# Performance work log

Measured on AMD Instinct MI355X. Metric: run time of the kernel, lower is better.

Reference implementation:

```python
import jax, jax.numpy as jnp
import numpy as np

M_TOKENS = 4096   # flattened batch*seq
K_IN = 4096       # in_features
N_OUT = 11008     # out_features
GROUPSIZE = 128


def setup_inputs() -> dict:
    key = jax.random.key(0)
    k1, k2, k3 = jax.random.split(key, 3)
    x = jax.random.normal(k1, (M_TOKENS, K_IN), dtype=jnp.float32)
    # unpacked int4 codes in [0, 15], row-major [N, K] (logical weight layout)
    weight_q = jax.random.randint(k2, (N_OUT, K_IN), 0, 16, dtype=jnp.int32)
    # [K//G, N, 2]: [..., 0] = scales, [..., 1] = zeros (gpt-fast pack_scales_and_zeros layout)
    scales_and_zeros = jax.random.uniform(k3, (K_IN // GROUPSIZE, N_OUT, 2), dtype=jnp.float32)
    return {"x": x, "weight_q": weight_q, "scales_and_zeros": scales_and_zeros}


def reference(x, weight_q, scales_and_zeros):
    # Group-wise affine dequant: w[k, n] = (q[n, k] - 8) * scale[k//G, n] + zero[k//G, n]
    N, K = weight_q.shape
    n_groups = scales_and_zeros.shape[0]
    G = K // n_groups
    scales = scales_and_zeros[..., 0]  # [K//G, N]
    zeros = scales_and_zeros[..., 1]   # [K//G, N]
    q = weight_q.astype(x.dtype).T.reshape(n_groups, G, N)          # [K//G, G, N]
    w = (q - 8.0) * scales[:, None, :] + zeros[:, None, :]          # [K//G, G, N]
    w = w.reshape(K, N)
    return x @ w  # [M, N]
```

## Files before the change

kernel.cpp:

```cpp
#include <hip/hip_runtime.h>
#include <hip/hip_bf16.h>
#include <math.h>

#define M_TOKENS 4096
#define K_IN     4096
#define N_OUT    11008

#define BM 256
#define BN 256
#define BK 128
#define KTILES (K_IN / BK)

typedef int i32x4 __attribute__((ext_vector_type(4)));

__device__ __forceinline__ void async_copy16(const void* g, void* l) {
    __builtin_amdgcn_global_load_lds(
        (const __attribute__((address_space(1))) void*)g,
        (__attribute__((address_space(3))) void*)l, 16, 0, 0);
}

__global__ __launch_bounds__(256) void quant_x_kernel(const float* __restrict__ x,
                                                      char* __restrict__ xq,
                                                      float* __restrict__ xs) {
    __shared__ float wmax[4];
    const int m = blockIdx.x;
    const int t = threadIdx.x;
    const float* row = x + (size_t)m * K_IN;
    float4 v[4];
    float lmax = 0.f;
#pragma unroll
    for (int p = 0; p < 4; ++p) {
        v[p] = *reinterpret_cast<const float4*>(row + p * 1024 + t * 4);
        lmax = fmaxf(lmax, fmaxf(fmaxf(fabsf(v[p].x), fabsf(v[p].y)),
                                 fmaxf(fabsf(v[p].z), fabsf(v[p].w))));
    }
#pragma unroll
    for (int off = 32; off >= 1; off >>= 1)
        lmax = fmaxf(lmax, __shfl_xor(lmax, off, 64));
    if ((t & 63) == 0) wmax[t >> 6] = lmax;
    __syncthreads();
    float gmax = fmaxf(fmaxf(wmax[0], wmax[1]), fmaxf(wmax[2], wmax[3]));
    gmax = fmaxf(gmax, 1e-20f);
    const float inv = 127.f / gmax;
    if (t == 0) xs[m] = gmax / 127.f;
#pragma unroll
    for (int p = 0; p < 4; ++p) {
        float vv[4] = {v[p].x, v[p].y, v[p].z, v[p].w};
        alignas(4) char c[4];
#pragma unroll
        for (int j = 0; j < 4; ++j) {
            float q = rintf(vv[j] * inv);
            q = fminf(fmaxf(q, -127.f), 127.f);
            c[j] = (char)(int)q;
        }
        *reinterpret_cast<unsigned*>(xq + (size_t)m * K_IN + p * 1024 + t * 4) =
            *reinterpret_cast<const unsigned*>(c);
    }
}

__global__ __launch_bounds__(256) void scale_w_kernel(const float* __restrict__ snz,
                                                      float* __restrict__ ws,
                                                      float* __restrict__ wsinv) {
    int n = blockIdx.x * 256 + threadIdx.x;
    if (n >= N_OUT) return;
    float m = 0.f;
#pragma unroll 4
    for (int g = 0; g < 32; ++g) {
        float s = snz[((size_t)g * N_OUT + n) * 2];
        float z = snz[((size_t)g * N_OUT + n) * 2 + 1];
        m = fmaxf(m, fmaxf(fabsf(z - 8.f * s), fabsf(z + 7.f * s)));
    }
    m = fmaxf(m, 1e-20f);
    ws[n] = m / 127.f;
    wsinv[n] = 127.f / m;
}

__global__ __launch_bounds__(256) void dequant_kernel(const int* __restrict__ wq,
                                                      const float* __restrict__ snz,
                                                      const float* __restrict__ wsinv,
                                                      char* __restrict__ wb) {
    size_t idx = (size_t)blockIdx.x * 256 + threadIdx.x;
    int n  = (int)(idx >> 9);
    int k8 = (int)(idx & 511);
    int g  = k8 >> 4;
    const float* sz = snz + ((size_t)g * N_OUT + n) * 2;
    float scale = sz[0], zero = sz[1];
    float inv = wsinv[n];
    const int4* q4 = reinterpret_cast<const int4*>(wq + (size_t)n * K_IN + (size_t)k8 * 8);
    int4 qa = q4[0], qb = q4[1];
    int q[8] = {qa.x, qa.y, qa.z, qa.w, qb.x, qb.y, qb.z, qb.w};
    alignas(8) char t[8];
#pragma unroll
    for (int j = 0; j < 8; ++j) {
        float w = (float)(q[j] - 8) * scale + zero;
        float qq = rintf(w * inv);
        qq = fminf(fmaxf(qq, -127.f), 127.f);
        t[j] = (char)(int)qq;
    }
    *reinterpret_cast<uint2*>(wb + idx * 8) = *reinterpret_cast<const uint2*>(t);
}


#define SCB()  __builtin_amdgcn_sched_barrier(0)
#define SBAR() { SCB(); __builtin_amdgcn_s_barrier(); SCB(); }
#define LGKM0() { asm volatile("s_waitcnt lgkmcnt(0)" ::: "memory"); SCB(); }
#define VM4()  { asm volatile("s_waitcnt vmcnt(4)" ::: "memory"); SCB(); }

#define RD_AL(T, S) \
    _Pragma("unroll") for (int mi = 0; mi < 4; ++mi) aL[mi] = readA(T, mi, S);
#define RD_AH(T, S) \
    _Pragma("unroll") for (int mi = 0; mi < 4; ++mi) aH[mi] = readA(T, 4 + mi, S);
#define RD_B4(T, S) \
    _Pragma("unroll") for (int ni = 0; ni < 4; ++ni) bk[ni] = readB(T, ni, S);

#define MFMA16(AOFF, FRAG) \
    __builtin_amdgcn_s_setprio(1); \
    { \
        _Pragma("unroll") for (int mi = 0; mi < 4; ++mi) \
        _Pragma("unroll") for (int ni = 0; ni < 4; ++ni) \
            acc[AOFF + mi][ni] = __builtin_amdgcn_mfma_i32_16x16x64_i8( \
                FRAG[mi], bk[ni], acc[AOFF + mi][ni], 0, 0, 0); \
    } \
    __builtin_amdgcn_s_setprio(0);

#define TILE(CA, CB, NA, NB, K1, K2) \
     \
    RD_AL(CA, 0); RD_B4(CB, 0); \
    stageB(NB, K1, 1); \
    SBAR(); LGKM0(); \
    MFMA16(0, aL); \
    VM4(); SBAR();    \
     \
    RD_AH(CA, 0); \
    stageA(NA, K1, 0); \
    SBAR(); LGKM0(); \
    MFMA16(4, aH); \
    SBAR(); \
     \
    RD_AL(CA, 1); RD_B4(CB, 1); \
    stageA(NA, K1, 1); \
    SBAR(); LGKM0(); \
    MFMA16(0, aL); \
    SBAR(); \
     \
    RD_AH(CA, 1); \
    stageB(CB, K2, 0); \
    SBAR(); LGKM0(); \
    MFMA16(4, aH); \
    VM4(); SBAR();

__global__ __launch_bounds__(512, 2) void gemm_i8_kernel(
        const char* __restrict__ Xq,
        const char* __restrict__ Wq,
        const float* __restrict__ xs,
        const float* __restrict__ ws,
        float* __restrict__ C) {
    __shared__ alignas(16) char smem[131072];
    char* const ldsA = smem;
    char* const ldsB = smem + 65536;

    const int tid  = threadIdx.x;
    const int lane = tid & 63;
    const int wave = tid >> 6;
    const int wr   = wave >> 2;
    const int wc   = wave & 3;
    const int l15  = lane & 15;
    const int lrow = lane >> 3;
    const int ssw  = (((lane & 7) ^ lrow) << 4);

    unsigned bid = blockIdx.x;
    unsigned per = gridDim.x >> 3;
    unsigned swz = (bid & 7u) * per + (bid >> 3);
    const int tn = (int)(swz % (N_OUT / BN));
    const int tm = (int)(swz / (N_OUT / BN));
    const int m0 = tm * BM;
    const int n0 = tn * BN;

    const int colswz = (((lane >> 4) << 4) ^ ((lane & 7) << 4));

    i32x4 acc[8][4];
#pragma unroll
    for (int i = 0; i < 8; ++i)
#pragma unroll
        for (int j = 0; j < 4; ++j) {
            i32x4 z = {0, 0, 0, 0};
            acc[i][j] = z;
        }
    i32x4 aL[4], aH[4], bk[4];

    auto stageA = [&](char* dstTile, int kt, int unit) {
#pragma unroll
        for (int j = 0; j < 2; ++j) {
            int c  = wave * 2 + j;
            int rb = (c >> 3) * 128 + (c & 7) * 8 + unit * 64;
            const char* g = Xq + (size_t)(m0 + rb + lrow) * K_IN
                            + (size_t)kt * 128 + ssw;
            async_copy16(g, dstTile + rb * 128);
        }
    };
    auto stageB = [&](char* dstTile, int kt, int unit) {
#pragma unroll
        for (int j = 0; j < 2; ++j) {
            int c  = wave * 2 + j;
            int rb = (c >> 2) * 64 + (c & 3) * 8 + unit * 32;
            const char* g = Wq + (size_t)(n0 + rb + lrow) * K_IN
                            + (size_t)kt * 128 + ssw;
            async_copy16(g, dstTile + rb * 128);
        }
    };
    auto readA = [&](char* tile, int mi8, int s) -> i32x4 {
        return *(const i32x4*)(tile + (wr * 128 + mi8 * 16 + l15) * 128 + (colswz ^ (s << 6)));
    };
    auto readB = [&](char* tile, int ni4, int s) -> i32x4 {
        return *(const i32x4*)(tile + (wc * 64 + ni4 * 16 + l15) * 128 + (colswz ^ (s << 6)));
    };

    char* const A0 = ldsA;   char* const A1 = ldsA + 32768;
    char* const B0 = ldsB;   char* const B1 = ldsB + 32768;

    stageB(B0, 0, 0); stageB(B0, 0, 1); stageA(A0, 0, 0); stageA(A0, 0, 1);
    stageB(B1, 1, 0);
    VM4(); SBAR();

    for (int i = 0; i < KTILES / 2; ++i) {
        const int k1 = (2 * i + 1) & (KTILES - 1);
        const int k2 = (2 * i + 2) & (KTILES - 1);
        const int k3 = (2 * i + 3) & (KTILES - 1);
        TILE(A0, B0, A1, B1, k1, k2)
        TILE(A1, B1, A0, B0, k2, k3)
    }

    const int r4 = (lane >> 4) << 2;
    float sn[4];
#pragma unroll
    for (int nf = 0; nf < 4; ++nf) sn[nf] = ws[n0 + wc * 64 + nf * 16 + l15];
#pragma unroll
    for (int mi = 0; mi < 8; ++mi) {
        const float4 xm = *reinterpret_cast<const float4*>(xs + m0 + wr * 128 + mi * 16 + r4);
        const float xv[4] = {xm.x, xm.y, xm.z, xm.w};
#pragma unroll
        for (int nf = 0; nf < 4; ++nf)
#pragma unroll
            for (int e = 0; e < 4; ++e) {
                int row = m0 + wr * 128 + mi * 16 + r4 + e;
                int col = n0 + wc * 64 + nf * 16 + l15;
                C[(size_t)row * N_OUT + col] = (float)acc[mi][nf][e] * xv[e] * sn[nf];
            }
    }
}

extern "C" void kernel_launch(void* const* d_in, const int* in_sizes, int n_in,
                              void* d_out, int out_size, void* d_ws, size_t ws_size,
                              hipStream_t stream) {
    const float* x   = (const float*)d_in[0];
    const int*   wq  = (const int*)d_in[1];
    const float* snz = (const float*)d_in[2];
    float* out = (float*)d_out;

    char*  Xq    = (char*)d_ws;
    char*  Wq8   = (char*)d_ws + ((size_t)M_TOKENS * K_IN);
    float* xs    = (float*)((char*)d_ws + (size_t)M_TOKENS * K_IN + (size_t)N_OUT * K_IN);
    float* ws    = xs + M_TOKENS;
    float* wsinv = ws + N_OUT;

    quant_x_kernel<<<M_TOKENS, 256, 0, stream>>>(x, Xq, xs);
    scale_w_kernel<<<(N_OUT + 255) / 256, 256, 0, stream>>>(snz, ws, wsinv);
    dequant_kernel<<<((size_t)N_OUT * K_IN) / 8 / 256, 256, 0, stream>>>(wq, snz, wsinv, Wq8);
    gemm_i8_kernel<<<(M_TOKENS / BM) * (N_OUT / BN), 512, 0, stream>>>(Xq, Wq8, xs, ws, out);
}
```

Before: 248.6 us.

## Shrink GEMM tile to 128x256 with single-buffered LDS and 4 waves

Reworks the int8 GEMM from a 256x256 tile with 8 waves and a hand-interleaved double-buffered pipeline into a 128x256 tile with 4 waves. Each wave now computes a 64x128 sub-tile. The kernel stages one K tile into a single LDS buffer, then loads fragments and runs all MFMAs before restaging the next tile. The smaller LDS footprint and block size may let more blocks share a CU and doubles the grid, but the code no longer overlaps global loads with MFMA inside a block, and per-tile data reuse drops.

```diff
diff --git a/kernel.cpp b/kernel.cpp
--- a/kernel.cpp
+++ b/kernel.cpp
@@ -6,7 +6,7 @@
 #define K_IN     4096
 #define N_OUT    11008
 
-#define BM 256
+#define BM 128
 #define BN 256
 #define BK 128
 #define KTILES (K_IN / BK)
@@ -103,67 +103,24 @@
 
 #define SCB()  __builtin_amdgcn_sched_barrier(0)
 #define SBAR() { SCB(); __builtin_amdgcn_s_barrier(); SCB(); }
-#define LGKM0() { asm volatile("s_waitcnt lgkmcnt(0)" ::: "memory"); SCB(); }
-#define VM4()  { asm volatile("s_waitcnt vmcnt(4)" ::: "memory"); SCB(); }
-
-#define RD_AL(T, S) \
-    _Pragma("unroll") for (int mi = 0; mi < 4; ++mi) aL[mi] = readA(T, mi, S);
-#define RD_AH(T, S) \
-    _Pragma("unroll") for (int mi = 0; mi < 4; ++mi) aH[mi] = readA(T, 4 + mi, S);
-#define RD_B4(T, S) \
-    _Pragma("unroll") for (int ni = 0; ni < 4; ++ni) bk[ni] = readB(T, ni, S);
-
-#define MFMA16(AOFF, FRAG) \
-    __builtin_amdgcn_s_setprio(1); \
-    { \
-        _Pragma("unroll") for (int mi = 0; mi < 4; ++mi) \
-        _Pragma("unroll") for (int ni = 0; ni < 4; ++ni) \
-            acc[AOFF + mi][ni] = __builtin_amdgcn_mfma_i32_16x16x64_i8( \
-                FRAG[mi], bk[ni], acc[AOFF + mi][ni], 0, 0, 0); \
-    } \
-    __builtin_amdgcn_s_setprio(0);
-
-#define TILE(CA, CB, NA, NB, K1, K2) \
-     \
-    RD_AL(CA, 0); RD_B4(CB, 0); \
-    stageB(NB, K1, 1); \
-    SBAR(); LGKM0(); \
-    MFMA16(0, aL); \
-    VM4(); SBAR();    \
-     \
-    RD_AH(CA, 0); \
-    stageA(NA, K1, 0); \
-    SBAR(); LGKM0(); \
-    MFMA16(4, aH); \
-    SBAR(); \
-     \
-    RD_AL(CA, 1); RD_B4(CB, 1); \
-    stageA(NA, K1, 1); \
-    SBAR(); LGKM0(); \
-    MFMA16(0, aL); \
-    SBAR(); \
-     \
-    RD_AH(CA, 1); \
-    stageB(CB, K2, 0); \
-    SBAR(); LGKM0(); \
-    MFMA16(4, aH); \
-    VM4(); SBAR();
-
-__global__ __launch_bounds__(512, 2) void gemm_i8_kernel(
+#define VM0BAR() { SCB(); asm volatile("s_waitcnt vmcnt(0)" ::: "memory"); \
+                   __builtin_amdgcn_s_barrier(); SCB(); }
+
+__global__ __launch_bounds__(256, 2) void gemm_i8_kernel(
         const char* __restrict__ Xq,
         const char* __restrict__ Wq,
         const float* __restrict__ xs,
         const float* __restrict__ ws,
         float* __restrict__ C) {
-    __shared__ alignas(16) char smem[131072];
+    __shared__ alignas(16) char smem[49152];
     char* const ldsA = smem;
-    char* const ldsB = smem + 65536;
+    char* const ldsB = smem + 16384;
 
     const int tid  = threadIdx.x;
     const int lane = tid & 63;
     const int wave = tid >> 6;
-    const int wr   = wave >> 2;
-    const int wc   = wave & 3;
+    const int wr   = wave >> 1;
+    const int wc   = wave & 1;
     const int l15  = lane & 15;
     const int lrow = lane >> 3;
     const int ssw  = (((lane & 7) ^ lrow) << 4);
@@ -178,73 +135,76 @@
 
     const int colswz = (((lane >> 4) << 4) ^ ((lane & 7) << 4));
 
-    i32x4 acc[8][4];
-#pragma unroll
-    for (int i = 0; i < 8; ++i)
-#pragma unroll
-        for (int j = 0; j < 4; ++j) {
+    i32x4 acc[4][8];
+#pragma unroll
+    for (int i = 0; i < 4; ++i)
+#pragma unroll
+        for (int j = 0; j < 8; ++j) {
             i32x4 z = {0, 0, 0, 0};
             acc[i][j] = z;
         }
-    i32x4 aL[4], aH[4], bk[4];
-
-    auto stageA = [&](char* dstTile, int kt, int unit) {
-#pragma unroll
-        for (int j = 0; j < 2; ++j) {
-            int c  = wave * 2 + j;
-            int rb = (c >> 3) * 128 + (c & 7) * 8 + unit * 64;
-            const char* g = Xq + (size_t)(m0 + rb + lrow) * K_IN
-                            + (size_t)kt * 128 + ssw;
-            async_copy16(g, dstTile + rb * 128);
+
+    auto stage = [&](int kt) {
+#pragma unroll
+        for (int j = 0; j < 4; ++j) {
+            int rm = j * 32 + wave * 8 + lrow;
+            const char* g = Xq + (size_t)(m0 + rm) * K_IN + (size_t)kt * 128 + ssw;
+            async_copy16(g, ldsA + rm * 128);
+        }
+#pragma unroll
+        for (int j = 0; j < 8; ++j) {
+            int rn = j * 32 + wave * 8 + lrow;
+            const char* g = Wq + (size_t)(n0 + rn) * K_IN + (size_t)kt * 128 + ssw;
+            async_copy16(g, ldsB + rn * 128);
         }
     };
-    auto stageB = [&](char* dstTile, int kt, int unit) {
-#pragma unroll
-        for (int j = 0; j < 2; ++j) {
-            int c  = wave * 2 + j;
-            int rb = (c >> 2) * 64 + (c & 3) * 8 + unit * 32;
-            const char* g = Wq + (size_t)(n0 + rb + lrow) * K_IN
-                            + (size_t)kt * 128 + ssw;
-            async_copy16(g, dstTile + rb * 128);
-        }
+    auto readA = [&](int mi, int s) -> i32x4 {
+        return *(const i32x4*)(ldsA + (wr * 64 + mi * 16 + l15) * 128 + (colswz ^ (s << 6)));
     };
-    auto readA = [&](char* tile, int mi8, int s) -> i32x4 {
-        return *(const i32x4*)(tile + (wr * 128 + mi8 * 16 + l15) * 128 + (colswz ^ (s << 6)));
+    auto readB = [&](int ni, int s) -> i32x4 {
+        return *(const i32x4*)(ldsB + (wc * 128 + ni * 16 + l15) * 128 + (colswz ^ (s << 6)));
     };
-    auto readB = [&](char* tile, int ni4, int s) -> i32x4 {
-        return *(const i32x4*)(tile + (wc * 64 + ni4 * 16 + l15) * 128 + (colswz ^ (s << 6)));
-    };
-
-    char* const A0 = ldsA;   char* const A1 = ldsA + 32768;
-    char* const B0 = ldsB;   char* const B1 = ldsB + 32768;
-
-    stageB(B0, 0, 0); stageB(B0, 0, 1); stageA(A0, 0, 0); stageA(A0, 0, 1);
-    stageB(B1, 1, 0);
-    VM4(); SBAR();
-
-    for (int i = 0; i < KTILES / 2; ++i) {
-        const int k1 = (2 * i + 1) & (KTILES - 1);
-        const int k2 = (2 * i + 2) & (KTILES - 1);
-        const int k3 = (2 * i + 3) & (KTILES - 1);
-        TILE(A0, B0, A1, B1, k1, k2)
-        TILE(A1, B1, A0, B0, k2, k3)
+
+    stage(0);
+    VM0BAR();
+
+    for (int t = 0; t < KTILES; ++t) {
+#pragma unroll
+        for (int s = 0; s < 2; ++s) {
+            i32x4 aF[4], bF[8];
+#pragma unroll
+            for (int mi = 0; mi < 4; ++mi) aF[mi] = readA(mi, s);
+#pragma unroll
+            for (int ni = 0; ni < 8; ++ni) bF[ni] = readB(ni, s);
+            __builtin_amdgcn_s_setprio(1);
+#pragma unroll
+            for (int mi = 0; mi < 4; ++mi)
+#pragma unroll
+                for (int ni = 0; ni < 8; ++ni)
+                    acc[mi][ni] = __builtin_amdgcn_mfma_i32_16x16x64_i8(
+                        aF[mi], bF[ni], acc[mi][ni], 0, 0, 0);
+            __builtin_amdgcn_s_setprio(0);
+        }
+        SBAR();
+        stage((t + 1) & (KTILES - 1));
+        VM0BAR();
     }
 
     const int r4 = (lane >> 4) << 2;
-    float sn[4];
-#pragma unroll
-    for (int nf = 0; nf < 4; ++nf) sn[nf] = ws[n0 + wc * 64 + nf * 16 + l15];
-#pragma unroll
-    for (int mi = 0; mi < 8; ++mi) {
-        const float4 xm = *reinterpret_cast<const float4*>(xs + m0 + wr * 128 + mi * 16 + r4);
+    float sn[8];
+#pragma unroll
+    for (int ni = 0; ni < 8; ++ni) sn[ni] = ws[n0 + wc * 128 + ni * 16 + l15];
+#pragma unroll
+    for (int mi = 0; mi < 4; ++mi) {
+        const float4 xm = *reinterpret_cast<const float4*>(xs + m0 + wr * 64 + mi * 16 + r4);
         const float xv[4] = {xm.x, xm.y, xm.z, xm.w};
 #pragma unroll
-        for (int nf = 0; nf < 4; ++nf)
+        for (int ni = 0; ni < 8; ++ni)
 #pragma unroll
             for (int e = 0; e < 4; ++e) {
-                int row = m0 + wr * 128 + mi * 16 + r4 + e;
-                int col = n0 + wc * 64 + nf * 16 + l15;
-                C[(size_t)row * N_OUT + col] = (float)acc[mi][nf][e] * xv[e] * sn[nf];
+                int row = m0 + wr * 64 + mi * 16 + r4 + e;
+                int col = n0 + wc * 128 + ni * 16 + l15;
+                C[(size_t)row * N_OUT + col] = (float)acc[mi][ni][e] * xv[e] * sn[ni];
             }
     }
 }
@@ -266,5 +226,5 @@
     quant_x_kernel<<<M_TOKENS, 256, 0, stream>>>(x, Xq, xs);
     scale_w_kernel<<<(N_OUT + 255) / 256, 256, 0, stream>>>(snz, ws, wsinv);
     dequant_kernel<<<((size_t)N_OUT * K_IN) / 8 / 256, 256, 0, stream>>>(wq, snz, wsinv, Wq8);
-    gemm_i8_kernel<<<(M_TOKENS / BM) * (N_OUT / BN), 512, 0, stream>>>(Xq, Wq8, xs, ws, out);
-}
+    gemm_i8_kernel<<<(M_TOKENS / BM) * (N_OUT / BN), 256, 0, stream>>>(Xq, Wq8, xs, ws, out);
+}
```

Result: slower. 299.9 us (+20.6%).
